# Performance work log

Measured on AMD Instinct MI355X. Metric: run time of the kernel, lower is better.

## Reference

```python
import jax, jax.numpy as jnp
import numpy as np

MASK_FILL = -1e9  # masked_fill_value (avoids NaNs vs -inf)

def setup_inputs() -> dict:
    key = jax.random.key(0)
    k1, k2, k3 = jax.random.split(key, 3)
    B, L, H, E = 4, 2048, 16, 128
    S, D = L, E
    queries = jax.random.normal(k1, (B, L, H, E), dtype=jnp.float32)
    keys = jax.random.normal(k2, (B, S, H, E), dtype=jnp.float32)
    values = jax.random.normal(k3, (B, S, H, D), dtype=jnp.float32)
    return {"queries": queries, "keys": keys, "values": values}

def reference(queries, keys, values):
    B, L, H, E = queries.shape
    S = keys.shape[1]
    scale = 1.0 / jnp.sqrt(jnp.asarray(E, queries.dtype))
    # compute_scores: dot-product scores (B,H,L,S)
    scores = jnp.einsum('blhe,bshe->bhls', queries, keys)
    # causal mask (mask_flag=True, attn_mask=None -> TriangularCausalMask)
    causal = jnp.triu(jnp.ones((L, S), dtype=bool), k=1)  # True above diagonal = masked
    scores = jnp.where(causal[None, None, :, :], MASK_FILL, scores)
    # scale * scores -> softmax (dropout p=0, eval)
    A = jax.nn.softmax(scale * scores, axis=-1)
    # combine_values: (B,H,L,S) x (B,S,H,D) -> (B,L,H,D)
    V = jnp.einsum('bhls,bshd->blhd', A, values)
    return V
```

## Files before the change

kernel.cpp:

```cpp
#include <hip/hip_runtime.h>
#include <hip/hip_bf16.h>

typedef __attribute__((ext_vector_type(4))) float f32x4;
typedef __attribute__((ext_vector_type(2))) float f32x2v;
typedef __attribute__((ext_vector_type(16))) float f32x16;
typedef __attribute__((ext_vector_type(8))) short s16x8;
typedef __attribute__((ext_vector_type(4))) short s16x4;
typedef __attribute__((ext_vector_type(4))) unsigned u32x4v;
typedef __attribute__((ext_vector_type(2))) int i32x2;

static constexpr int Bb = 4, Ll = 2048, Hh = 16, Ee = 128;
static constexpr int RS = Hh * Ee;
static constexpr float SCALE = 0.088388347648318447f;
static constexpr float LOG2E = 1.4426950408889634f;
static constexpr float SCL = SCALE * LOG2E;
static constexpr float MOFF = 26.0f;

static constexpr int KROW = 272;
static constexpr int KBYTES = 32 * KROW;
static constexpr int VROW = 80;
static constexpr int VBYTES = 128 * VROW;
static constexpr int BUFSZ = KBYTES + VBYTES;

__device__ __forceinline__ unsigned pk2bf(float lo, float hi) {
  float2 t = make_float2(lo, hi);
  __hip_bfloat162 b2 = __float22bfloat162_rn(t);
  union { __hip_bfloat162 b; unsigned u; } cv; cv.b = b2;
  return cv.u;
}

__device__ __forceinline__ s16x8 pack8(float a0, float a1, float a2, float a3,
                                       float a4, float a5, float a6, float a7) {
  u32x4v u = { pk2bf(a0,a1), pk2bf(a2,a3), pk2bf(a4,a5), pk2bf(a6,a7) };
  return *(s16x8*)&u;
}

__device__ __forceinline__ void plswap(int &x, int &y, int h5) {
#if __has_builtin(__builtin_amdgcn_permlane32_swap)
  i32x2 r = __builtin_amdgcn_permlane32_swap(x, y, false, false);
  x = r[0]; y = r[1];
#else
  int px = __shfl_xor(x, 32, 64);
  int py = __shfl_xor(y, 32, 64);
  int nx = h5 ? py : x;
  int ny = h5 ? y : px;
  x = nx; y = ny;
#endif
}

__device__ __forceinline__ s16x8 mkpa(float p0, float p1, float p2, float p3,
                                      float p4, float p5, float p6, float p7, int h5) {
  int uA = (int)pk2bf(p0, p1), uB = (int)pk2bf(p2, p3);
  int uC = (int)pk2bf(p4, p5), uD = (int)pk2bf(p6, p7);
  plswap(uA, uC, h5);
  plswap(uB, uD, h5);
  u32x4v u = { (unsigned)uA, (unsigned)uB, (unsigned)uC, (unsigned)uD };
  return *(s16x8*)&u;
}

__device__ __forceinline__ void gl_lds16(const short* g, short* l) {
  __builtin_amdgcn_global_load_lds((const __attribute__((address_space(1))) void*)g,
                                   (__attribute__((address_space(3))) void*)l, 16, 0, 0);
}

__global__ __launch_bounds__(256) void conv_k(const float* __restrict__ src, short* __restrict__ dst) {
  size_t i = ((size_t)blockIdx.x * 256 + threadIdx.x) * 8;
  f32x4 a = *(const f32x4*)(src + i);
  f32x4 b = *(const f32x4*)(src + i + 4);
  *(s16x8*)(dst + i) = pack8(a[0],a[1],a[2],a[3],b[0],b[1],b[2],b[3]);
}

__global__ __launch_bounds__(256) void conv_vt(const float* __restrict__ V, unsigned* __restrict__ Vt32) {
  const int bh = blockIdx.x >> 4, s0 = (blockIdx.x & 15) * 128;
  const int b = bh >> 4, h = bh & 15;
  const int w = threadIdx.x >> 6, lane = threadIdx.x & 63;
  const float* base = V + ((size_t)(b * Ll + s0 + 32 * w)) * RS + h * Ee + 2 * lane;
  unsigned w0[16], w1[16];
#pragma unroll
  for (int j = 0; j < 16; ++j) {
    f32x2v a = *(const f32x2v*)(base + (size_t)(2 * j) * RS);
    f32x2v c = *(const f32x2v*)(base + (size_t)(2 * j + 1) * RS);
    w0[j] = pk2bf(a[0], c[0]);
    w1[j] = pk2bf(a[1], c[1]);
  }
  unsigned* r0 = Vt32 + ((size_t)(bh * 128 + 2 * lane)) * 1024 + (s0 + 32 * w) / 2;
  unsigned* r1 = r0 + 1024;
#pragma unroll
  for (int jj = 0; jj < 4; ++jj) {
    *(u32x4v*)(r0 + 4 * jj) = (u32x4v){w0[4*jj], w0[4*jj+1], w0[4*jj+2], w0[4*jj+3]};
    *(u32x4v*)(r1 + 4 * jj) = (u32x4v){w1[4*jj], w1[4*jj+1], w1[4*jj+2], w1[4*jj+3]};
  }
}

__global__ __launch_bounds__(256, 2)
void attn_main(const float* __restrict__ Qg, const short* __restrict__ Kws,
               const short* __restrict__ Vtws, float* __restrict__ Og) {
  const int phys = blockIdx.x;
  const int qi = ((phys >> 6) & 1) ? (phys >> 7) : (15 - (phys >> 7));
  const int bh = phys & 63;
  const int b = bh >> 4, h = bh & 15;
  const int qb = qi * 128;
  const int tid = threadIdx.x, w = tid >> 6, l = tid & 63;
  const int l31 = l & 31, h5 = l >> 5;

  __shared__ __align__(16) short smem[2 * BUFSZ];

  s16x8 qfrag[8];
  {
    const float* qp = Qg + ((size_t)(b * Ll + qb + 32 * w + l31)) * RS + h * Ee;
#pragma unroll
    for (int ks = 0; ks < 8; ++ks) {
      const int e0 = 16 * ks + 8 * h5;
      f32x4 f0 = *(const f32x4*)(qp + e0);
      f32x4 f1 = *(const f32x4*)(qp + e0 + 4);
      qfrag[ks] = pack8(f0[0]*SCL, f0[1]*SCL, f0[2]*SCL, f0[3]*SCL,
                        f1[0]*SCL, f1[1]*SCL, f1[2]*SCL, f1[3]*SCL);
    }
  }

  f32x16 acc[4];
#pragma unroll
  for (int dt = 0; dt < 4; ++dt)
#pragma unroll
    for (int r = 0; r < 16; ++r) acc[dt][r] = 0.f;
  float lacc = 0.f;

  const short* skp[3]; const short* svp[3];
  int kdst[3], vdst[3];
#pragma unroll
  for (int j = 0; j < 3; ++j) {
    const int kid = (j < 2) ? (w * 136 + 64 * j + l) : (w * 136 + 128 + (l & 7));
    const int kr = kid / 17;
    int ksl = kid % 17; if (ksl == 16) ksl = 0;
    skp[j] = Kws + ((size_t)(b * Ll + kr)) * 2048 + h * 128 + ksl * 8;
    kdst[j] = kid * 16;
    const int vid = (j < 2) ? (w * 160 + 64 * j + l) : (w * 160 + 128 + (l & 31));
    const int vr = vid / 5;
    int vsl = vid % 5; if (vsl == 4) vsl = 0;
    svp[j] = Vtws + ((size_t)(bh * 128 + vr)) * 2048 + vsl * 8;
    vdst[j] = KBYTES + vid * 16;
  }

#define STAGE(cb, kvb) do { \
    gl_lds16(skp[0] + (size_t)(kvb) * 2048, (short*)((char*)smem + (cb) + kdst[0])); \
    gl_lds16(skp[1] + (size_t)(kvb) * 2048, (short*)((char*)smem + (cb) + kdst[1])); \
    if (l < 8)  gl_lds16(skp[2] + (size_t)(kvb) * 2048, (short*)((char*)smem + (cb) + kdst[2])); \
    gl_lds16(svp[0] + (kvb), (short*)((char*)smem + (cb) + vdst[0])); \
    gl_lds16(svp[1] + (kvb), (short*)((char*)smem + (cb) + vdst[1])); \
    if (l < 32) gl_lds16(svp[2] + (kvb), (short*)((char*)smem + (cb) + vdst[2])); \
  } while (0)

  const int ntiles = 4 * qi + 4;
  const int tmaxw = 4 * qi + w;

  STAGE(0, 0);
  STAGE(BUFSZ, 32);

  for (int t = 0; t < ntiles; ++t) {
    const int cbase = (t & 3) * BUFSZ;
    if (t + 2 < ntiles) {
      STAGE(((t + 2) & 3) * BUFSZ, 32 * (t + 2));
      asm volatile("s_waitcnt vmcnt(12)" ::: "memory");
    } else if (t + 2 == ntiles) {
      asm volatile("s_waitcnt vmcnt(6)" ::: "memory");
    } else {
      asm volatile("s_waitcnt vmcnt(0)" ::: "memory");
    }
    __builtin_amdgcn_s_barrier();
    __builtin_amdgcn_sched_barrier(0);

    if (t <= tmaxw) {
      f32x16 s;
#pragma unroll
      for (int r = 0; r < 16; ++r) s[r] = 0.f;
      __builtin_amdgcn_s_setprio(1);
#pragma unroll
      for (int ks = 0; ks < 8; ++ks) {
        s16x8 a = *(const s16x8*)((const char*)smem + cbase + l31 * KROW + h5 * 16 + ks * 32);
        s = __builtin_amdgcn_mfma_f32_32x32x16_bf16(a, qfrag[ks], s, 0, 0, 0);
      }
      __builtin_amdgcn_s_setprio(0);

      if (t == tmaxw) {
#pragma unroll
        for (int r = 0; r < 16; ++r) {
          const int kvl = (r & 3) + 8 * (r >> 2) + 4 * h5;
          if (kvl > l31) s[r] = -3.0e38f;
        }
      }

      float pv[16];
#pragma unroll
      for (int r = 0; r < 16; ++r) { const float p2 = exp2f(s[r] - MOFF); pv[r] = p2; lacc += p2; }
      s16x8 pa0 = mkpa(pv[0], pv[1], pv[2], pv[3], pv[4], pv[5], pv[6], pv[7], h5);
      s16x8 pa1 = mkpa(pv[8], pv[9], pv[10], pv[11], pv[12], pv[13], pv[14], pv[15], h5);

      __builtin_amdgcn_s_setprio(1);
#pragma unroll
      for (int dt = 0; dt < 4; ++dt) {
        const int vb = cbase + KBYTES + dt * (32 * VROW) + l31 * VROW + h5 * 16;
        s16x8 av0 = *(const s16x8*)((const char*)smem + vb);
        acc[dt] = __builtin_amdgcn_mfma_f32_32x32x16_bf16(av0, pa0, acc[dt], 0, 0, 0);
        s16x8 av1 = *(const s16x8*)((const char*)smem + vb + 32);
        acc[dt] = __builtin_amdgcn_mfma_f32_32x32x16_bf16(av1, pa1, acc[dt], 0, 0, 0);
      }
      __builtin_amdgcn_s_setprio(0);
    }
    __builtin_amdgcn_sched_barrier(0);
  }
#undef STAGE

  float lsum;
  {
    int pb = __builtin_bit_cast(int, lacc), pc = pb;
    plswap(pb, pc, h5);
    lsum = __builtin_bit_cast(float, pb) + __builtin_bit_cast(float, pc);
  }
  const float linv = 1.0f / lsum;

  float* orow = Og + ((size_t)(b * Ll + qb + 32 * w + l31)) * RS + h * Ee;
#pragma unroll
  for (int dt = 0; dt < 4; ++dt)
#pragma unroll
    for (int g = 0; g < 4; ++g) {
      f32x4 v = { acc[dt][4*g] * linv, acc[dt][4*g+1] * linv,
                  acc[dt][4*g+2] * linv, acc[dt][4*g+3] * linv };
      *(f32x4*)(orow + dt * 32 + g * 8 + h5 * 4) = v;
    }
}

static constexpr int VPAD = 66;
__device__ __forceinline__ short f2bf(float f) {
  union { float f; unsigned u; } x; x.f = f;
  unsigned r = x.u + 0x7FFFu + ((x.u >> 16) & 1u);
  return (short)(r >> 16);
}
__global__ __launch_bounds__(256, 4)
void attn_fwd(const float* __restrict__ Qg, const float* __restrict__ Kg,
              const float* __restrict__ Vg, float* __restrict__ Og) {
  const int qi = blockIdx.x;
  const int bh = blockIdx.y;
  const int b = bh >> 4, h = bh & 15;
  const int qb = qi * 64;
  const int tid = threadIdx.x, wave = tid >> 6, lane = tid & 63, lo = lane & 15, hi = lane >> 4;
  __shared__ __align__(16) short Klds[64 * 128];
  __shared__ __align__(16) short Vt[128 * VPAD];
  const float* Qb_ = Qg + (size_t)b * Ll * RS + h * Ee;
  const float* Kb_ = Kg + (size_t)b * Ll * RS + h * Ee;
  const float* Vb_ = Vg + (size_t)b * Ll * RS + h * Ee;
  float* Ob_ = Og + (size_t)b * Ll * RS + h * Ee;
  s16x8 qfrag[4];
  {
    const float* qp = Qb_ + (size_t)(qb + wave * 16 + lo) * RS;
#pragma unroll
    for (int ks = 0; ks < 4; ++ks) {
      const int e0 = 32 * ks + 8 * hi;
      f32x4 f0 = *(const f32x4*)(qp + e0);
      f32x4 f1 = *(const f32x4*)(qp + e0 + 4);
      qfrag[ks] = pack8(f0[0]*SCALE, f0[1]*SCALE, f0[2]*SCALE, f0[3]*SCALE,
                        f1[0]*SCALE, f1[1]*SCALE, f1[2]*SCALE, f1[3]*SCALE);
    }
  }
  f32x4 acc[8];
#pragma unroll
  for (int nt = 0; nt < 8; ++nt) acc[nt] = (f32x4){0.f, 0.f, 0.f, 0.f};
  float mrun = -3.0e38f, lrun = 0.f;
  const int r0 = tid >> 4, c0 = (tid & 15) * 8;
  for (int kvb = 0; kvb <= qb; kvb += 64) {
    __syncthreads();
#pragma unroll
    for (int rr4 = 0; rr4 < 4; ++rr4) {
      const int rr = r0 + 16 * rr4;
      const float* kp = Kb_ + (size_t)(kvb + rr) * RS + c0;
      f32x4 f0 = *(const f32x4*)kp;
      f32x4 f1 = *(const f32x4*)(kp + 4);
      const int off = (rr * 256 + c0 * 2) ^ ((rr & 7) << 4);
      *(s16x8*)((char*)Klds + off) = pack8(f0[0],f0[1],f0[2],f0[3],f1[0],f1[1],f1[2],f1[3]);
    }
#pragma unroll
    for (int kk = 0; kk < 2; ++kk) {
      const int kv0 = (r0 * 2 + kk) * 2;
      const float* vp0 = Vb_ + (size_t)(kvb + kv0) * RS + c0;
      const float* vp1 = vp0 + RS;
      f32x4 a0 = *(const f32x4*)vp0, a1 = *(const f32x4*)(vp0 + 4);
      f32x4 b0 = *(const f32x4*)vp1, b1 = *(const f32x4*)(vp1 + 4);
#pragma unroll
      for (int jj = 0; jj < 4; ++jj)
        *(unsigned*)&Vt[(c0 + jj) * VPAD + kv0] = pk2bf(a0[jj], b0[jj]);
#pragma unroll
      for (int jj = 0; jj < 4; ++jj)
        *(unsigned*)&Vt[(c0 + 4 + jj) * VPAD + kv0] = pk2bf(a1[jj], b1[jj]);
    }
    __syncthreads();
    const bool diag = (kvb == qb);
    f32x4 st[4];
#pragma unroll
    for (int mt = 0; mt < 4; ++mt) {
      f32x4 a4 = (f32x4){0.f, 0.f, 0.f, 0.f};
#pragma unroll
      for (int ks = 0; ks < 4; ++ks) {
        const int row = 16 * mt + lo;
        const int off = (row * 256 + (32 * ks + 8 * hi) * 2) ^ ((row & 7) << 4);
        s16x8 a = *(const s16x8*)((const char*)Klds + off);
        a4 = __builtin_amdgcn_mfma_f32_16x16x32_bf16(a, qfrag[ks], a4, 0, 0, 0);
      }
      st[mt] = a4;
    }
    if (diag) {
      const int qg = 16 * wave + lo;
#pragma unroll
      for (int mt = 0; mt < 4; ++mt)
#pragma unroll
        for (int r = 0; r < 4; ++r)
          if (16 * mt + 4 * hi + r > qg) st[mt][r] = -3.0e38f;
    }
    float mx = -3.0e38f;
#pragma unroll
    for (int mt = 0; mt < 4; ++mt)
#pragma unroll
      for (int r = 0; r < 4; ++r) mx = fmaxf(mx, st[mt][r]);
    mx = fmaxf(mx, __shfl_xor(mx, 16, 64));
    mx = fmaxf(mx, __shfl_xor(mx, 32, 64));
    const float mnew = fmaxf(mrun, mx);
    const float alpha = exp2f((mrun - mnew) * LOG2E);
    float psum = 0.f;
    s16x4 pf[4];
#pragma unroll
    for (int mt = 0; mt < 4; ++mt)
#pragma unroll
      for (int r = 0; r < 4; ++r) {
        const float p = exp2f((st[mt][r] - mnew) * LOG2E);
        psum += p;
        pf[mt][r] = f2bf(p);
      }
    psum += __shfl_xor(psum, 16, 64);
    psum += __shfl_xor(psum, 32, 64);
    lrun = lrun * alpha + psum;
    mrun = mnew;
    float alr[4];
#pragma unroll
    for (int r = 0; r < 4; ++r) alr[r] = __shfl(alpha, 4 * hi + r, 64);
#pragma unroll
    for (int nt = 0; nt < 8; ++nt) {
      acc[nt][0] *= alr[0]; acc[nt][1] *= alr[1];
      acc[nt][2] *= alr[2]; acc[nt][3] *= alr[3];
    }
#pragma unroll
    for (int mt = 0; mt < 4; ++mt)
#pragma unroll
      for (int nt = 0; nt < 8; ++nt) {
        const int hw = (16 * nt + lo) * VPAD + 16 * mt + 4 * hi;
        s16x4 vf = *(const s16x4*)&Vt[hw];
        acc[nt] = __builtin_amdgcn_mfma_f32_16x16x16bf16_1k(pf[mt], vf, acc[nt], 0, 0, 0);
      }
  }
  float linv[4];
#pragma unroll
  for (int r = 0; r < 4; ++r) linv[r] = 1.0f / __shfl(lrun, 4 * hi + r, 64);
#pragma unroll
  for (int r = 0; r < 4; ++r) {
    const int qg = qb + 16 * wave + 4 * hi + r;
    float* op = Ob_ + (size_t)qg * RS + lo;
#pragma unroll
    for (int nt = 0; nt < 8; ++nt)
      op[16 * nt] = acc[nt][r] * linv[r];
  }
}

extern "C" void kernel_launch(void* const* d_in, const int* in_sizes, int n_in,
                              void* d_out, int out_size, void* d_ws, size_t ws_size,
                              hipStream_t stream) {
  const float* Qp = (const float*)d_in[0];
  const float* Kp = (const float*)d_in[1];
  const float* Vp = (const float*)d_in[2];
  float* Op = (float*)d_out;
  const size_t elems = (size_t)Bb * Ll * Hh * Ee;
  if (ws_size >= elems * 2 * 2) {
    short* Kws = (short*)d_ws;
    short* Vtws = Kws + elems;
    conv_k<<<(int)(elems / 8 / 256), 256, 0, stream>>>(Kp, Kws);
    conv_vt<<<Bb * Hh * (Ll / 128), 256, 0, stream>>>(Vp, (unsigned*)Vtws);
    attn_main<<<1024, 256, 0, stream>>>(Qp, Kws, Vtws, Op);
  } else {
    dim3 grid(Ll / 64, Bb * Hh);
    attn_fwd<<<grid, 256, 0, stream>>>(Qp, Kp, Vp, Op);
  }
}
```

Before: 169.4 us.

## Software-pipeline QK^T of next tile with PV of current tile

Restructures the attention main loop so that each iteration computes QK^T for tile t+1 and the PV product for tile t. The softmax/exp of one tile can then overlap with the MFMAs of the other, reducing the serial dependency between score computation and value accumulation. It adds a prologue and epilogue and changes the vmcnt waits so K of the next tile is resident one step earlier, at the cost of extra live registers for the carried P fragments.

```diff
diff --git a/kernel.cpp b/kernel.cpp
--- a/kernel.cpp
+++ b/kernel.cpp
@@ -150,18 +150,60 @@
     if (l < 32) gl_lds16(svp[2] + (kvb), (short*)((char*)smem + (cb) + vdst[2])); \
   } while (0)
 
+#define QKT(kb, sreg) do { \
+    _Pragma("unroll") for (int r = 0; r < 16; ++r) (sreg)[r] = 0.f; \
+    _Pragma("unroll") for (int ks = 0; ks < 8; ++ks) { \
+      s16x8 a_ = *(const s16x8*)((const char*)smem + (kb) + l31 * KROW + h5 * 16 + ks * 32); \
+      (sreg) = __builtin_amdgcn_mfma_f32_32x32x16_bf16(a_, qfrag[ks], (sreg), 0, 0, 0); \
+    } \
+  } while (0)
+
+#define PVOP(vb_) do { \
+    _Pragma("unroll") for (int dt = 0; dt < 4; ++dt) { \
+      const int vbb = (vb_) + KBYTES + dt * (32 * VROW) + l31 * VROW + h5 * 16; \
+      s16x8 av0 = *(const s16x8*)((const char*)smem + vbb); \
+      acc[dt] = __builtin_amdgcn_mfma_f32_32x32x16_bf16(av0, pa0, acc[dt], 0, 0, 0); \
+      s16x8 av1 = *(const s16x8*)((const char*)smem + vbb + 32); \
+      acc[dt] = __builtin_amdgcn_mfma_f32_32x32x16_bf16(av1, pa1, acc[dt], 0, 0, 0); \
+    } \
+  } while (0)
+
+#define SMAX(sreg) do { \
+    float pv_[16]; \
+    _Pragma("unroll") for (int r = 0; r < 16; ++r) { \
+      const float p2_ = exp2f((sreg)[r] - MOFF); pv_[r] = p2_; lacc += p2_; } \
+    pa0 = mkpa(pv_[0],pv_[1],pv_[2],pv_[3],pv_[4],pv_[5],pv_[6],pv_[7], h5); \
+    pa1 = mkpa(pv_[8],pv_[9],pv_[10],pv_[11],pv_[12],pv_[13],pv_[14],pv_[15], h5); \
+  } while (0)
+
+#define MASK(sreg) do { \
+    _Pragma("unroll") for (int r = 0; r < 16; ++r) { \
+      const int kvl_ = (r & 3) + 8 * (r >> 2) + 4 * h5; \
+      if (kvl_ > l31) (sreg)[r] = -3.0e38f; } \
+  } while (0)
+
   const int ntiles = 4 * qi + 4;
   const int tmaxw = 4 * qi + w;
 
   STAGE(0, 0);
   STAGE(BUFSZ, 32);
 
-  for (int t = 0; t < ntiles; ++t) {
-    const int cbase = (t & 3) * BUFSZ;
+  s16x8 pa0, pa1;
+  asm volatile("s_waitcnt vmcnt(6)" ::: "memory");
+  __builtin_amdgcn_s_barrier();
+  __builtin_amdgcn_sched_barrier(0);
+  {
+    f32x16 s;
+    QKT(0, s);
+    if (0 == tmaxw) MASK(s);
+    SMAX(s);
+  }
+
+  for (int t = 0; t < ntiles - 1; ++t) {
+    const int vbuf = (t & 3) * BUFSZ;
+    const int kbuf = ((t + 1) & 3) * BUFSZ;
     if (t + 2 < ntiles) {
       STAGE(((t + 2) & 3) * BUFSZ, 32 * (t + 2));
-      asm volatile("s_waitcnt vmcnt(12)" ::: "memory");
-    } else if (t + 2 == ntiles) {
       asm volatile("s_waitcnt vmcnt(6)" ::: "memory");
     } else {
       asm volatile("s_waitcnt vmcnt(0)" ::: "memory");
@@ -169,46 +211,29 @@
     __builtin_amdgcn_s_barrier();
     __builtin_amdgcn_sched_barrier(0);
 
-    if (t <= tmaxw) {
-      f32x16 s;
-#pragma unroll
-      for (int r = 0; r < 16; ++r) s[r] = 0.f;
-      __builtin_amdgcn_s_setprio(1);
-#pragma unroll
-      for (int ks = 0; ks < 8; ++ks) {
-        s16x8 a = *(const s16x8*)((const char*)smem + cbase + l31 * KROW + h5 * 16 + ks * 32);
-        s = __builtin_amdgcn_mfma_f32_32x32x16_bf16(a, qfrag[ks], s, 0, 0, 0);
-      }
-      __builtin_amdgcn_s_setprio(0);
-
-      if (t == tmaxw) {
-#pragma unroll
-        for (int r = 0; r < 16; ++r) {
-          const int kvl = (r & 3) + 8 * (r >> 2) + 4 * h5;
-          if (kvl > l31) s[r] = -3.0e38f;
-        }
-      }
-
-      float pv[16];
-#pragma unroll
-      for (int r = 0; r < 16; ++r) { const float p2 = exp2f(s[r] - MOFF); pv[r] = p2; lacc += p2; }
-      s16x8 pa0 = mkpa(pv[0], pv[1], pv[2], pv[3], pv[4], pv[5], pv[6], pv[7], h5);
-      s16x8 pa1 = mkpa(pv[8], pv[9], pv[10], pv[11], pv[12], pv[13], pv[14], pv[15], h5);
-
-      __builtin_amdgcn_s_setprio(1);
-#pragma unroll
-      for (int dt = 0; dt < 4; ++dt) {
-        const int vb = cbase + KBYTES + dt * (32 * VROW) + l31 * VROW + h5 * 16;
-        s16x8 av0 = *(const s16x8*)((const char*)smem + vb);
-        acc[dt] = __builtin_amdgcn_mfma_f32_32x32x16_bf16(av0, pa0, acc[dt], 0, 0, 0);
-        s16x8 av1 = *(const s16x8*)((const char*)smem + vb + 32);
-        acc[dt] = __builtin_amdgcn_mfma_f32_32x32x16_bf16(av1, pa1, acc[dt], 0, 0, 0);
-      }
-      __builtin_amdgcn_s_setprio(0);
+    const bool doQ = (t + 1 <= tmaxw);
+    const bool doP = (t <= tmaxw);
+    f32x16 s;
+    __builtin_amdgcn_s_setprio(1);
+    if (doQ) QKT(kbuf, s);
+    if (doP) PVOP(vbuf);
+    __builtin_amdgcn_s_setprio(0);
+    if (doQ) {
+      if (t + 1 == tmaxw) MASK(s);
+      SMAX(s);
     }
     __builtin_amdgcn_sched_barrier(0);
   }
+
+  if (tmaxw == ntiles - 1) {
+    const int vbuf = ((ntiles - 1) & 3) * BUFSZ;
+    PVOP(vbuf);
+  }
 #undef STAGE
+#undef QKT
+#undef PVOP
+#undef SMAX
+#undef MASK
 
   float lsum;
   {
```

New measurement: 167.8 us. About the same (-0.9%).
